# Optimization experiments

Hardware: AMD Instinct MI355X
Metric: run time of the kernel (lower is better)

The kernel has to match this reference:

```python
import jax, jax.numpy as jnp
import numpy as np

B, S, D = 8, 4096, 768
HEADS = 12
NEIGHBORS = 2
DILATION = 1
KERNEL = 1 + 2 * NEIGHBORS  # 5
DIM_HEAD = D // HEADS


def setup_inputs() -> dict:
    key = jax.random.key(0)
    ks = jax.random.split(key, 11)
    sc = 1.0 / np.sqrt(D)
    return {
        "x": jax.random.normal(ks[0], (B, S, D), dtype=jnp.float32),
        "Wq": jax.random.normal(ks[1], (D, D), dtype=jnp.float32) * sc,
        "bq": jax.random.normal(ks[2], (D,), dtype=jnp.float32) * 0.02,
        "Wk": jax.random.normal(ks[3], (D, D), dtype=jnp.float32) * sc,
        "bk": jax.random.normal(ks[4], (D,), dtype=jnp.float32) * 0.02,
        "Wv": jax.random.normal(ks[5], (D, D), dtype=jnp.float32) * sc,
        "bv": jax.random.normal(ks[6], (D,), dtype=jnp.float32) * 0.02,
        "Wo": jax.random.normal(ks[7], (D, D), dtype=jnp.float32) * sc,
        "bo": jax.random.normal(ks[8], (D,), dtype=jnp.float32) * 0.02,
        "gamma": jnp.ones((D,), dtype=jnp.float32),
        "beta": jnp.zeros((D,), dtype=jnp.float32),
    }


def _extract_seq_patches(x, kernel_size, dilation):
    # [B, S, D] -> [B, S, kernel_size, D] of dilated local windows, zero-padded.
    seq_len = x.shape[1]
    patch_size = kernel_size + (dilation - 1) * (kernel_size - 1)
    pad_r = (patch_size - 1) // 2
    pad_l = patch_size - pad_r - 1
    xp = jnp.pad(x, ((0, 0), (pad_l, pad_r), (0, 0)))
    # small fixed loop over kernel positions (kernel_size = 5)
    return jnp.stack([xp[:, i:i + seq_len] for i in range(0, patch_size, dilation)], axis=2)


def reference(x, Wq, bq, Wk, bk, Wv, bv, Wo, bo, gamma, beta):
    patches = _extract_seq_patches(x, KERNEL, DILATION)  # [B, S, K, D]
    q = x @ Wq + bq                                       # [B, S, D]
    k = patches @ Wk + bk                                 # [B, S, K, D]
    v = patches @ Wv + bv                                 # [B, S, K, D]
    # split heads
    q = q.reshape(B, S, HEADS, DIM_HEAD)
    k = k.reshape(B, S, KERNEL, HEADS, DIM_HEAD)
    v = v.reshape(B, S, KERNEL, HEADS, DIM_HEAD)
    scale = jnp.sqrt(jnp.asarray(DIM_HEAD, dtype=q.dtype))
    scores = jnp.einsum('bshd,bskhd->bshk', q, k) / scale  # [B, S, H, K]
    p = jax.nn.softmax(scores, axis=-1)
    att = jnp.einsum('bshk,bskhd->bshd', p, v)             # [B, S, H, dh]
    att = att.reshape(B, S, D)
    att = att @ Wo + bo
    y = att + x
    # LayerNorm over last dim
    mu = jnp.mean(y, axis=-1, keepdims=True)
    var = jnp.var(y, axis=-1, keepdims=True)
    y = (y - mu) / jnp.sqrt(var + 1e-5) * gamma + beta
    return y
```

## Files before the change

### kernel.cpp

```cpp
#include <hip/hip_runtime.h>

#define B_  8
#define S_  4096
#define D_  768
#define H_  12
#define M_  (B_ * S_)
#define NQKV_ 2304

typedef unsigned short u16;
typedef __attribute__((ext_vector_type(4))) float  f32x4;
typedef __attribute__((ext_vector_type(8))) __bf16 bf16x8;
typedef __attribute__((ext_vector_type(4))) u16    u16x4;

#define GAS __attribute__((address_space(1)))
#define LAS __attribute__((address_space(3)))

__device__ __forceinline__ u16 f2bf(float f) {
    unsigned u = __float_as_uint(f);
    u += 0x7FFF + ((u >> 16) & 1);
    return (u16)(u >> 16);
}
__device__ __forceinline__ float bf2f(u16 h) {
    return __uint_as_float(((unsigned)h) << 16);
}

__device__ __forceinline__ void gload_lds16(const void* g, void* l) {
    __builtin_amdgcn_global_load_lds((const GAS void*)g, (LAS void*)l, 16, 0, 0);
}

__device__ __forceinline__ int xcd_swz(int bid, int nwg) {
    return (bid & 7) * (nwg >> 3) + (bid >> 3);
}

__global__ __launch_bounds__(256) void castx_kernel(const float* __restrict__ x,
                                                    u16* __restrict__ xb) {
    const int i = blockIdx.x * 256 + threadIdx.x;
    const float4 v = ((const float4*)x)[i];
    u16x4 o;
    o.x = f2bf(v.x); o.y = f2bf(v.y); o.z = f2bf(v.z); o.w = f2bf(v.w);
    ((u16x4*)xb)[i] = o;
}

__global__ __launch_bounds__(256) void wtrans_kernel(const float* __restrict__ Wq,
                                                     const float* __restrict__ Wk,
                                                     const float* __restrict__ Wv,
                                                     const float* __restrict__ Wo,
                                                     u16* __restrict__ Wb) {
    const float* W = (blockIdx.z == 0) ? Wq : (blockIdx.z == 1) ? Wk
                   : (blockIdx.z == 2) ? Wv : Wo;
    u16* O = Wb + (size_t)blockIdx.z * D_ * D_;
    __shared__ float tile[32][33];
    const int tx = threadIdx.x & 31, ty = threadIdx.x >> 5;
    const int k0 = blockIdx.y * 32, n0 = blockIdx.x * 32;
#pragma unroll
    for (int j = 0; j < 4; j++)
        tile[ty + j * 8][tx] = W[(size_t)(k0 + ty + j * 8) * D_ + n0 + tx];
    __syncthreads();
#pragma unroll
    for (int j = 0; j < 4; j++)
        O[(size_t)(n0 + ty + j * 8) * D_ + k0 + tx] = f2bf(tile[tx][ty + j * 8]);
}

template <int MODE>
__global__ __launch_bounds__(256) void gemm_kernel(
    const u16* __restrict__ A, const u16* __restrict__ Wb,
    const float* __restrict__ b0, const float* __restrict__ b1,
    const float* __restrict__ b2,
    u16* __restrict__ outb, float* __restrict__ outf,
    const float* __restrict__ xres) {
    __shared__ u16 Als[128 * 32];
    __shared__ u16 Bls[128 * 32];

    const int t = threadIdx.x;
    const int w = t >> 6, l = t & 63;
    const int NX = (MODE == 0) ? 18 : 6;
    const int work = xcd_swz(blockIdx.x, gridDim.x);
    const int bx = work % NX;
    const int m0 = (work / NX) * 128;
    int widx, nloc;
    if (MODE == 0) { widx = bx / 6; nloc = bx % 6; }
    else           { widx = 3;      nloc = bx;     }
    const int n0 = nloc * 128;
    const u16* Bt = Wb + (size_t)widx * (D_ * D_);
    const float* bias = (MODE == 0) ? (widx == 0 ? b0 : widx == 1 ? b1 : b2) : b0;

    const int srow  = t >> 2;
    const int sbyte = (t & 3) * 16;
    const char* Ag = (const char*)(A  + (size_t)(m0 + srow) * D_) + sbyte;
    const char* Bg = (const char*)(Bt + (size_t)(n0 + srow) * D_) + sbyte;
    char* Al = (char*)Als + w * 1024;
    char* Bl = (char*)Bls + w * 1024;

    f32x4 acc[4][4];
#pragma unroll
    for (int i = 0; i < 4; i++)
#pragma unroll
        for (int j = 0; j < 4; j++) acc[i][j] = (f32x4){0.f, 0.f, 0.f, 0.f};

    const int mbase = (w >> 1) * 64, nbase = (w & 1) * 64;
    const int fr   = l & 15;
    const int koff = (l >> 4) * 8;

    for (int kt = 0; kt < D_; kt += 32) {
        const int cb = kt * 2;
        gload_lds16(Ag + cb,                 Al);
        gload_lds16(Ag + cb + 64 * (D_ * 2), Al + 4096);
        gload_lds16(Bg + cb,                 Bl);
        gload_lds16(Bg + cb + 64 * (D_ * 2), Bl + 4096);
        __syncthreads();

        bf16x8 af[4], bf[4];
#pragma unroll
        for (int mi = 0; mi < 4; mi++)
            af[mi] = *(const bf16x8*)(Als + (mbase + mi * 16 + fr) * 32 + koff);
#pragma unroll
        for (int ni = 0; ni < 4; ni++)
            bf[ni] = *(const bf16x8*)(Bls + (nbase + ni * 16 + fr) * 32 + koff);
#pragma unroll
        for (int mi = 0; mi < 4; mi++)
#pragma unroll
            for (int ni = 0; ni < 4; ni++)
                acc[mi][ni] = __builtin_amdgcn_mfma_f32_16x16x32_bf16(
                    af[mi], bf[ni], acc[mi][ni], 0, 0, 0);
        __syncthreads();
    }

    const int crow0 = m0 + mbase + (l >> 4) * 4;
    const int ccol0 = nbase + fr;
    if (MODE == 0) {
        const int cbase = widx * D_ + n0;
#pragma unroll
        for (int mi = 0; mi < 4; mi++)
#pragma unroll
            for (int ni = 0; ni < 4; ni++) {
                const int cc = ccol0 + ni * 16;
                const float bv = bias[n0 + cc];
#pragma unroll
                for (int r = 0; r < 4; r++)
                    outb[(size_t)(crow0 + mi * 16 + r) * NQKV_ + cbase + cc] =
                        f2bf(acc[mi][ni][r] + bv);
            }
    } else {
#pragma unroll
        for (int mi = 0; mi < 4; mi++)
#pragma unroll
            for (int ni = 0; ni < 4; ni++) {
                const int cc = n0 + ccol0 + ni * 16;
                const float bv = bias[cc];
#pragma unroll
                for (int r = 0; r < 4; r++) {
                    const size_t idx = (size_t)(crow0 + mi * 16 + r) * D_ + cc;
                    outf[idx] = acc[mi][ni][r] + bv + xres[idx];
                }
            }
    }
}

__global__ __launch_bounds__(256) void attn_kernel(const u16* __restrict__ QKV,
                                                   const float* __restrict__ bk,
                                                   const float* __restrict__ bv,
                                                   u16* __restrict__ att) {
    const int gw = xcd_swz(blockIdx.x, gridDim.x) * 4 + (threadIdx.x >> 6);
    const int l  = threadIdx.x & 63;
    const int hq = gw % 3;
    const int m  = gw / 3;
    const int s  = m & (S_ - 1);
    const int col = hq * 256 + l * 4;
    const u16* base = QKV + (size_t)m * NQKV_;

    const u16x4 qv = *(const u16x4*)(base + col);
    float qf[4];
#pragma unroll
    for (int j = 0; j < 4; j++) qf[j] = bf2f(qv[j]);

    float sc[5];
#pragma unroll
    for (int i = 0; i < 5; i++) {
        const int sp = s + i - 2;
        float p;
        if (sp >= 0 && sp < S_) {
            const u16x4 kv = *(const u16x4*)(base + (i - 2) * NQKV_ + D_ + col);
            p = qf[0] * bf2f(kv[0]) + qf[1] * bf2f(kv[1])
              + qf[2] * bf2f(kv[2]) + qf[3] * bf2f(kv[3]);
        } else {
            const float4 kb = *(const float4*)(bk + col);
            p = qf[0] * kb.x + qf[1] * kb.y + qf[2] * kb.z + qf[3] * kb.w;
        }
#pragma unroll
        for (int off = 1; off < 16; off <<= 1) p += __shfl_xor(p, off, 64);
        sc[i] = p * 0.125f;
    }
    float mx = sc[0];
#pragma unroll
    for (int i = 1; i < 5; i++) mx = fmaxf(mx, sc[i]);
    float e[5], sum = 0.f;
#pragma unroll
    for (int i = 0; i < 5; i++) { e[i] = __expf(sc[i] - mx); sum += e[i]; }
    const float inv = 1.f / sum;

    float o[4] = {0.f, 0.f, 0.f, 0.f};
#pragma unroll
    for (int i = 0; i < 5; i++) {
        const float wgt = e[i] * inv;
        const int sp = s + i - 2;
        if (sp >= 0 && sp < S_) {
            const u16x4 vv = *(const u16x4*)(base + (i - 2) * NQKV_ + 2 * D_ + col);
#pragma unroll
            for (int j = 0; j < 4; j++) o[j] += wgt * bf2f(vv[j]);
        } else {
            const float4 vb = *(const float4*)(bv + col);
            o[0] += wgt * vb.x; o[1] += wgt * vb.y;
            o[2] += wgt * vb.z; o[3] += wgt * vb.w;
        }
    }
    u16x4 ov;
#pragma unroll
    for (int j = 0; j < 4; j++) ov[j] = f2bf(o[j]);
    *(u16x4*)(att + (size_t)m * D_ + col) = ov;
}

__global__ __launch_bounds__(256) void ln_kernel(const float* __restrict__ Y,
                                                 const float* __restrict__ gamma,
                                                 const float* __restrict__ beta,
                                                 float* __restrict__ out) {
    const int row = blockIdx.x;
    const float* r = Y + (size_t)row * D_;
    const int t = threadIdx.x;
    const float v0 = r[t], v1 = r[t + 256], v2 = r[t + 512];
    float s  = v0 + v1 + v2;
    float s2 = v0 * v0 + v1 * v1 + v2 * v2;
#pragma unroll
    for (int off = 32; off > 0; off >>= 1) {
        s  += __shfl_xor(s,  off, 64);
        s2 += __shfl_xor(s2, off, 64);
    }
    __shared__ float red[8];
    const int w = t >> 6, l = t & 63;
    if (l == 0) { red[w] = s; red[4 + w] = s2; }
    __syncthreads();
    s  = red[0] + red[1] + red[2] + red[3];
    s2 = red[4] + red[5] + red[6] + red[7];
    const float mu  = s * (1.f / 768.f);
    const float var = s2 * (1.f / 768.f) - mu * mu;
    const float inv = rsqrtf(var + 1e-5f);
    float* o = out + (size_t)row * D_;
    o[t]       = (v0 - mu) * inv * gamma[t]       + beta[t];
    o[t + 256] = (v1 - mu) * inv * gamma[t + 256] + beta[t + 256];
    o[t + 512] = (v2 - mu) * inv * gamma[t + 512] + beta[t + 512];
}

extern "C" void kernel_launch(void* const* d_in, const int* in_sizes, int n_in,
                              void* d_out, int out_size, void* d_ws, size_t ws_size,
                              hipStream_t stream) {
    const float* x     = (const float*)d_in[0];
    const float* Wq    = (const float*)d_in[1];
    const float* bq    = (const float*)d_in[2];
    const float* Wk    = (const float*)d_in[3];
    const float* bk    = (const float*)d_in[4];
    const float* Wv    = (const float*)d_in[5];
    const float* bv    = (const float*)d_in[6];
    const float* Wo    = (const float*)d_in[7];
    const float* bo    = (const float*)d_in[8];
    const float* gamma = (const float*)d_in[9];
    const float* beta  = (const float*)d_in[10];

    char* ws = (char*)d_ws;
    u16*   Wb  = (u16*)ws;
    u16*   xb  = (u16*)(ws + 4718592);
    u16*   QKV = (u16*)(ws + 4718592 + 50331648);
    float* yp  = (float*)QKV;
    u16*   att = xb;

    castx_kernel<<<(M_ * D_) / (256 * 4), 256, 0, stream>>>(x, xb);
    wtrans_kernel<<<dim3(24, 24, 4), 256, 0, stream>>>(Wq, Wk, Wv, Wo, Wb);
    gemm_kernel<0><<<18 * (M_ / 128), 256, 0, stream>>>(xb, Wb, bq, bk, bv,
                                                        QKV, nullptr, nullptr);
    attn_kernel<<<(M_ * 3) / 4, 256, 0, stream>>>(QKV, bk, bv, att);
    gemm_kernel<1><<<6 * (M_ / 128), 256, 0, stream>>>(att, Wb, bo, nullptr, nullptr,
                                                       nullptr, yp, x);
    ln_kernel<<<M_, 256, 0, stream>>>(yp, gamma, beta, (float*)d_out);
}
```

Baseline: 355.2 us.

## Replace GEMMs with 256x256 8-wave double-buffered pipelined MFMA kernel

Both projection GEMMs move from a 128x128, 4-wave, single-buffered loop to a 256x256, 8-wave kernel. It uses 128KB of dynamic LDS with double buffering, swizzled chunks to avoid bank conflicts, and interleaves global-to-LDS loads with MFMA quarters using explicit vmcnt waits and setprio. The output GEMM also switches to a bf16 residual (xb) and writes a bf16 pre-LN tensor, and the LN kernel now reads bf16 to halve that traffic. The gains are meant to come from higher arithmetic intensity and overlapped memory latency. The costs are lower precision on the residual and LN input, and occupancy limited by the large LDS footprint.

```diff
diff --git a/kernel.cpp b/kernel.cpp
--- a/kernel.cpp
+++ b/kernel.cpp
@@ -6,6 +6,7 @@
 #define H_  12
 #define M_  (B_ * S_)
 #define NQKV_ 2304
+#define NTILES 12
 
 typedef unsigned short u16;
 typedef __attribute__((ext_vector_type(4))) float  f32x4;
@@ -61,96 +62,176 @@
         O[(size_t)(n0 + ty + j * 8) * D_ + k0 + tx] = f2bf(tile[tx][ty + j * 8]);
 }
 
+
+#define SYNC_NOVM()                                          \
+    __builtin_amdgcn_sched_barrier(0);                       \
+    __builtin_amdgcn_s_barrier();                            \
+    asm volatile("s_waitcnt lgkmcnt(0)" ::: "memory");       \
+    __builtin_amdgcn_sched_barrier(0)
+
+#define SYNC_VM(N)                                           \
+    __builtin_amdgcn_sched_barrier(0);                       \
+    asm volatile("s_waitcnt vmcnt(" #N ")" ::: "memory");    \
+    __builtin_amdgcn_s_barrier();                            \
+    asm volatile("s_waitcnt lgkmcnt(0)" ::: "memory");       \
+    __builtin_amdgcn_sched_barrier(0)
+
+#define TRAIL()                                              \
+    __builtin_amdgcn_sched_barrier(0);                       \
+    __builtin_amdgcn_s_barrier()
+
+#define MFMA_Q(AF, BF, MO, NO)                                               \
+    __builtin_amdgcn_s_setprio(1);                                           \
+    _Pragma("unroll") for (int mi = 0; mi < 4; ++mi)                         \
+        _Pragma("unroll") for (int ni = 0; ni < 2; ++ni)                     \
+            _Pragma("unroll") for (int kh = 0; kh < 2; ++kh)                 \
+                acc[mi + MO][ni + NO] =                                      \
+                    __builtin_amdgcn_mfma_f32_16x16x32_bf16(                 \
+                        AF[mi][kh], BF[ni][kh], acc[mi + MO][ni + NO], 0, 0, 0); \
+    __builtin_amdgcn_s_setprio(0)
+
 template <int MODE>
-__global__ __launch_bounds__(256) void gemm_kernel(
+__global__ __launch_bounds__(512, 2) void gemm8_kernel(
     const u16* __restrict__ A, const u16* __restrict__ Wb,
     const float* __restrict__ b0, const float* __restrict__ b1,
     const float* __restrict__ b2,
-    u16* __restrict__ outb, float* __restrict__ outf,
-    const float* __restrict__ xres) {
-    __shared__ u16 Als[128 * 32];
-    __shared__ u16 Bls[128 * 32];
+    u16* __restrict__ outb, const u16* __restrict__ xres) {
+    extern __shared__ char lds[];
 
     const int t = threadIdx.x;
     const int w = t >> 6, l = t & 63;
-    const int NX = (MODE == 0) ? 18 : 6;
+    const int wm = w >> 2, wn = w & 3;
+
+    const int NTN = (MODE == 0) ? 9 : 3;
     const int work = xcd_swz(blockIdx.x, gridDim.x);
-    const int bx = work % NX;
-    const int m0 = (work / NX) * 128;
-    int widx, nloc;
-    if (MODE == 0) { widx = bx / 6; nloc = bx % 6; }
-    else           { widx = 3;      nloc = bx;     }
-    const int n0 = nloc * 128;
-    const u16* Bt = Wb + (size_t)widx * (D_ * D_);
-    const float* bias = (MODE == 0) ? (widx == 0 ? b0 : widx == 1 ? b1 : b2) : b0;
-
-    const int srow  = t >> 2;
-    const int sbyte = (t & 3) * 16;
-    const char* Ag = (const char*)(A  + (size_t)(m0 + srow) * D_) + sbyte;
-    const char* Bg = (const char*)(Bt + (size_t)(n0 + srow) * D_) + sbyte;
-    char* Al = (char*)Als + w * 1024;
-    char* Bl = (char*)Bls + w * 1024;
-
-    f32x4 acc[4][4];
-#pragma unroll
-    for (int i = 0; i < 4; i++)
+    const int mt = work / NTN, nt = work % NTN;
+    const int m0 = mt * 256;
+    const int n0 = nt * 256;
+    const int widx = (MODE == 0) ? (n0 / D_) : 3;
+    const int n0w = n0 - ((MODE == 0) ? widx * D_ : 0);
+
+    const int srow   = t >> 3;
+    const int schunk = (t & 7) ^ (srow & 7);
+    const u16* Asrc = A + (size_t)(m0 + srow) * D_ + schunk * 8;
+    const u16* Bsrc = Wb + (size_t)widx * (D_ * D_) + (size_t)(n0w + srow) * D_ + schunk * 8;
+
+    auto STAGE_A = [&](int h, int tk, int db) {
+        const u16* s = Asrc + (size_t)(h * 128) * D_ + tk * 64;
+        char* d = lds + db * 65536 + h * 16384 + (w << 10);
+        gload_lds16(s, d);
+        gload_lds16(s + 64 * D_, d + 8192);
+    };
+    auto STAGE_B = [&](int h, int tk, int db) {
+        const u16* s = Bsrc + (size_t)(h * 128) * D_ + tk * 64;
+        char* d = lds + db * 65536 + 32768 + h * 16384 + (w << 10);
+        gload_lds16(s, d);
+        gload_lds16(s + 64 * D_, d + 8192);
+    };
+
+    const int ck0 = (((l >> 4) ^ (l & 7)) << 4);
+    const int ck1 = ((((l >> 4) + 4) ^ (l & 7)) << 4);
+    const int aRowB = (wm * 128 + (l & 15)) * 128;
+    const int bRowB = 32768 + (wn * 64 + (l & 15)) * 128;
+#define LDSREAD(off) (*(const bf16x8*)(lds + (off)))
+
+    f32x4 acc[8][4];
+#pragma unroll
+    for (int i = 0; i < 8; i++)
 #pragma unroll
         for (int j = 0; j < 4; j++) acc[i][j] = (f32x4){0.f, 0.f, 0.f, 0.f};
 
-    const int mbase = (w >> 1) * 64, nbase = (w & 1) * 64;
-    const int fr   = l & 15;
-    const int koff = (l >> 4) * 8;
-
-    for (int kt = 0; kt < D_; kt += 32) {
-        const int cb = kt * 2;
-        gload_lds16(Ag + cb,                 Al);
-        gload_lds16(Ag + cb + 64 * (D_ * 2), Al + 4096);
-        gload_lds16(Bg + cb,                 Bl);
-        gload_lds16(Bg + cb + 64 * (D_ * 2), Bl + 4096);
-        __syncthreads();
-
-        bf16x8 af[4], bf[4];
-#pragma unroll
-        for (int mi = 0; mi < 4; mi++)
-            af[mi] = *(const bf16x8*)(Als + (mbase + mi * 16 + fr) * 32 + koff);
-#pragma unroll
-        for (int ni = 0; ni < 4; ni++)
-            bf[ni] = *(const bf16x8*)(Bls + (nbase + ni * 16 + fr) * 32 + koff);
-#pragma unroll
-        for (int mi = 0; mi < 4; mi++)
-#pragma unroll
-            for (int ni = 0; ni < 4; ni++)
-                acc[mi][ni] = __builtin_amdgcn_mfma_f32_16x16x32_bf16(
-                    af[mi], bf[ni], acc[mi][ni], 0, 0, 0);
-        __syncthreads();
-    }
-
-    const int crow0 = m0 + mbase + (l >> 4) * 4;
-    const int ccol0 = nbase + fr;
+    bf16x8 Alo[4][2], Ahi[4][2], Ba[2][2], Bb[2][2];
+
+    STAGE_A(0, 0, 0); STAGE_A(1, 0, 0); STAGE_B(0, 0, 0); STAGE_B(1, 0, 0);
+    STAGE_A(0, 1, 1); STAGE_A(1, 1, 1); STAGE_B(0, 1, 1);
+    __builtin_amdgcn_sched_barrier(0);
+    asm volatile("s_waitcnt vmcnt(6)" ::: "memory");
+    __builtin_amdgcn_s_barrier();
+#pragma unroll
+    for (int mi = 0; mi < 4; ++mi) {
+        Alo[mi][0] = LDSREAD(aRowB + mi * 2048 + ck0);
+        Alo[mi][1] = LDSREAD(aRowB + mi * 2048 + ck1);
+    }
+#pragma unroll
+    for (int ni = 0; ni < 2; ++ni) {
+        Ba[ni][0] = LDSREAD(bRowB + ni * 2048 + ck0);
+        Ba[ni][1] = LDSREAD(bRowB + ni * 2048 + ck1);
+    }
+
+    for (int X = 0; X < NTILES; ++X) {
+        const int bX = X & 1;
+        const int L0off = bX << 16;
+        const int L1off = (bX ^ 1) << 16;
+        int t1 = X + 1; if (t1 >= NTILES) t1 -= NTILES;
+        int t2 = X + 2; if (t2 >= NTILES) t2 -= NTILES;
+
+#pragma unroll
+        for (int mi = 0; mi < 4; ++mi) {
+            Ahi[mi][0] = LDSREAD(L0off + aRowB + (mi + 4) * 2048 + ck0);
+            Ahi[mi][1] = LDSREAD(L0off + aRowB + (mi + 4) * 2048 + ck1);
+        }
+#pragma unroll
+        for (int ni = 0; ni < 2; ++ni) {
+            Bb[ni][0] = LDSREAD(L0off + bRowB + (ni + 2) * 2048 + ck0);
+            Bb[ni][1] = LDSREAD(L0off + bRowB + (ni + 2) * 2048 + ck1);
+        }
+        STAGE_B(1, t1, bX ^ 1);
+        SYNC_NOVM();
+        MFMA_Q(Alo, Ba, 0, 0);
+        TRAIL();
+
+        STAGE_A(0, t2, bX);
+        SYNC_VM(6);
+        MFMA_Q(Alo, Bb, 0, 2);
+        TRAIL();
+
+#pragma unroll
+        for (int mi = 0; mi < 4; ++mi) {
+            Alo[mi][0] = LDSREAD(L1off + aRowB + mi * 2048 + ck0);
+            Alo[mi][1] = LDSREAD(L1off + aRowB + mi * 2048 + ck1);
+        }
+        STAGE_A(1, t2, bX);
+        SYNC_VM(4);
+        MFMA_Q(Ahi, Ba, 4, 0);
+        TRAIL();
+
+#pragma unroll
+        for (int ni = 0; ni < 2; ++ni) {
+            Ba[ni][0] = LDSREAD(L1off + bRowB + ni * 2048 + ck0);
+            Ba[ni][1] = LDSREAD(L1off + bRowB + ni * 2048 + ck1);
+        }
+        STAGE_B(0, t2, bX);
+        SYNC_VM(6);
+        MFMA_Q(Ahi, Bb, 4, 2);
+        TRAIL();
+    }
+
+    const int crow0 = m0 + wm * 128 + ((l >> 4) << 2);
+    const int ccol0 = n0 + wn * 64 + (l & 15);
     if (MODE == 0) {
-        const int cbase = widx * D_ + n0;
-#pragma unroll
-        for (int mi = 0; mi < 4; mi++)
-#pragma unroll
-            for (int ni = 0; ni < 4; ni++) {
-                const int cc = ccol0 + ni * 16;
-                const float bv = bias[n0 + cc];
-#pragma unroll
-                for (int r = 0; r < 4; r++)
-                    outb[(size_t)(crow0 + mi * 16 + r) * NQKV_ + cbase + cc] =
+        const float* bias = (widx == 0) ? b0 : (widx == 1) ? b1 : b2;
+        const int bcol0 = ccol0 - widx * D_;
+#pragma unroll
+        for (int mi = 0; mi < 8; ++mi)
+#pragma unroll
+            for (int ni = 0; ni < 4; ++ni) {
+                const float bv = bias[bcol0 + ni * 16];
+#pragma unroll
+                for (int r = 0; r < 4; ++r)
+                    outb[(size_t)(crow0 + mi * 16 + r) * NQKV_ + ccol0 + ni * 16] =
                         f2bf(acc[mi][ni][r] + bv);
             }
     } else {
 #pragma unroll
-        for (int mi = 0; mi < 4; mi++)
-#pragma unroll
-            for (int ni = 0; ni < 4; ni++) {
-                const int cc = n0 + ccol0 + ni * 16;
-                const float bv = bias[cc];
-#pragma unroll
-                for (int r = 0; r < 4; r++) {
-                    const size_t idx = (size_t)(crow0 + mi * 16 + r) * D_ + cc;
-                    outf[idx] = acc[mi][ni][r] + bv + xres[idx];
+        for (int mi = 0; mi < 8; ++mi)
+#pragma unroll
+            for (int ni = 0; ni < 4; ++ni) {
+                const int col = ccol0 + ni * 16;
+                const float bv = b0[col];
+#pragma unroll
+                for (int r = 0; r < 4; ++r) {
+                    const size_t idx = (size_t)(crow0 + mi * 16 + r) * D_ + col;
+                    outb[idx] = f2bf(acc[mi][ni][r] + bv + bf2f(xres[idx]));
                 }
             }
     }
@@ -219,14 +300,14 @@
     *(u16x4*)(att + (size_t)m * D_ + col) = ov;
 }
 
-__global__ __launch_bounds__(256) void ln_kernel(const float* __restrict__ Y,
+__global__ __launch_bounds__(256) void ln_kernel(const u16* __restrict__ Yb,
                                                  const float* __restrict__ gamma,
                                                  const float* __restrict__ beta,
                                                  float* __restrict__ out) {
     const int row = blockIdx.x;
-    const float* r = Y + (size_t)row * D_;
+    const u16* r = Yb + (size_t)row * D_;
     const int t = threadIdx.x;
-    const float v0 = r[t], v1 = r[t + 256], v2 = r[t + 512];
+    const float v0 = bf2f(r[t]), v1 = bf2f(r[t + 256]), v2 = bf2f(r[t + 512]);
     float s  = v0 + v1 + v2;
     float s2 = v0 * v0 + v1 * v1 + v2 * v2;
 #pragma unroll
@@ -268,15 +349,20 @@
     u16*   Wb  = (u16*)ws;
     u16*   xb  = (u16*)(ws + 4718592);
     u16*   QKV = (u16*)(ws + 4718592 + 50331648);
-    float* yp  = (float*)QKV;
-    u16*   att = xb;
+    u16*   yb  = QKV;
+    u16*   att = (u16*)d_out;
+
+    (void)hipFuncSetAttribute(reinterpret_cast<const void*>(&gemm8_kernel<0>),
+                              hipFuncAttributeMaxDynamicSharedMemorySize, 131072);
+    (void)hipFuncSetAttribute(reinterpret_cast<const void*>(&gemm8_kernel<1>),
+                              hipFuncAttributeMaxDynamicSharedMemorySize, 131072);
 
     castx_kernel<<<(M_ * D_) / (256 * 4), 256, 0, stream>>>(x, xb);
     wtrans_kernel<<<dim3(24, 24, 4), 256, 0, stream>>>(Wq, Wk, Wv, Wo, Wb);
-    gemm_kernel<0><<<18 * (M_ / 128), 256, 0, stream>>>(xb, Wb, bq, bk, bv,
-                                                        QKV, nullptr, nullptr);
+    gemm8_kernel<0><<<(M_ / 256) * 9, 512, 131072, stream>>>(xb, Wb, bq, bk, bv,
+                                                             QKV, nullptr);
     attn_kernel<<<(M_ * 3) / 4, 256, 0, stream>>>(QKV, bk, bv, att);
-    gemm_kernel<1><<<6 * (M_ / 128), 256, 0, stream>>>(att, Wb, bo, nullptr, nullptr,
-                                                       nullptr, yp, x);
-    ln_kernel<<<M_, 256, 0, stream>>>(yp, gamma, beta, (float*)d_out);
-}
+    gemm8_kernel<1><<<(M_ / 256) * 3, 512, 131072, stream>>>(att, Wb, bo, nullptr, nullptr,
+                                                             yb, xb);
+    ln_kernel<<<M_, 256, 0, stream>>>(yb, gamma, beta, (float*)d_out);
+}
```

New measurement: 354.1 us. Within noise of the previous version (-0.3%).
